# Kernel optimization log

Measured on AMD Instinct MI355X. Metric: run time of the kernel, lower is better.

The kernel has to match this reference:

```python
import jax, jax.numpy as jnp
import numpy as np

HIDDEN = 10

def setup_inputs() -> dict:
    key = jax.random.key(0)
    ks = jax.random.split(key, 12)
    B, T = 4096, 2048
    s_in = 1.0 / np.sqrt(HIDDEN)  # PyTorch RNN/Linear default init scale
    inp = {
        "x": jax.random.normal(ks[0], (B, T, 1), dtype=jnp.float32),
        "hidden_state": jax.random.normal(ks[1], (2, B, HIDDEN), dtype=jnp.float32),
        # layer 0 (input_size=1)
        "W_ih0": jax.random.uniform(ks[2], (HIDDEN, 1), jnp.float32, -s_in, s_in),
        "W_hh0": jax.random.uniform(ks[3], (HIDDEN, HIDDEN), jnp.float32, -s_in, s_in),
        "b_ih0": jax.random.uniform(ks[4], (HIDDEN,), jnp.float32, -s_in, s_in),
        "b_hh0": jax.random.uniform(ks[5], (HIDDEN,), jnp.float32, -s_in, s_in),
        # layer 1 (input_size=HIDDEN)
        "W_ih1": jax.random.uniform(ks[6], (HIDDEN, HIDDEN), jnp.float32, -s_in, s_in),
        "W_hh1": jax.random.uniform(ks[7], (HIDDEN, HIDDEN), jnp.float32, -s_in, s_in),
        "b_ih1": jax.random.uniform(ks[8], (HIDDEN,), jnp.float32, -s_in, s_in),
        "b_hh1": jax.random.uniform(ks[9], (HIDDEN,), jnp.float32, -s_in, s_in),
        # output Linear(10, 1)
        "W_out": jax.random.uniform(ks[10], (1, HIDDEN), jnp.float32, -s_in, s_in),
        "b_out": jax.random.uniform(ks[11], (1,), jnp.float32, -s_in, s_in),
    }
    return inp


def reference(x, hidden_state, W_ih0, W_hh0, b_ih0, b_hh0,
              W_ih1, W_hh1, b_ih1, b_hh1, W_out, b_out):
    # x: [B, T, 1]; hidden_state: [2, B, H]
    h0_init, h1_init = hidden_state[0], hidden_state[1]  # [B, H] each
    xs = jnp.swapaxes(x, 0, 1)  # [T, B, 1] for scan over time

    def step(carry, xt):
        h0, h1 = carry
        h0n = jnp.tanh(xt @ W_ih0.T + b_ih0 + h0 @ W_hh0.T + b_hh0)
        h1n = jnp.tanh(h0n @ W_ih1.T + b_ih1 + h1 @ W_hh1.T + b_hh1)
        return (h0n, h1n), h1n

    (h0_f, h1_f), ys = jax.lax.scan(step, (h0_init, h1_init), xs)  # ys: [T, B, H]
    rnn_output = jnp.swapaxes(ys, 0, 1)  # [B, T, H]
    outs = rnn_output @ W_out.T + b_out  # [B, T, 1] (fused per-timestep Linear)
    hidden_out = jnp.stack([h0_f, h1_f], axis=0)  # [2, B, H]
    return outs, hidden_out
```

## Files before the change

kernel.cpp:

```cpp
#include <hip/hip_runtime.h>

#define HID 10
#define TT  2048
#define BB  4096

typedef float f2 __attribute__((ext_vector_type(2)));

static __device__ __forceinline__ f2 pkmul(f2 a, f2 b) {
    f2 d; asm("v_pk_mul_f32 %0, %1, %2" : "=v"(d) : "v"(a), "v"(b)); return d;
}
static __device__ __forceinline__ f2 pkfma(f2 a, f2 b, f2 c) {
    f2 d; asm("v_pk_fma_f32 %0, %1, %2, %3" : "=v"(d) : "v"(a), "v"(b), "v"(c)); return d;
}

__device__ __forceinline__ float fast_tanh(float x) {
    float e = exp2f(x * 2.885390081777926814f);
    float r = __builtin_amdgcn_rcpf(e + 1.0f);
    return fmaf(-2.0f, r, 1.0f);
}

__global__ void __launch_bounds__(192) rnn_kernel(
    const float* __restrict__ x,    const float* __restrict__ hs,
    const float* __restrict__ Wih0, const float* __restrict__ Whh0,
    const float* __restrict__ bih0, const float* __restrict__ bhh0,
    const float* __restrict__ Wih1, const float* __restrict__ Whh1,
    const float* __restrict__ bih1, const float* __restrict__ bhh1,
    const float* __restrict__ Wout, const float* __restrict__ boutp,
    float* __restrict__ out)
{
    const int tid   = threadIdx.x;
    const int role  = tid >> 6;
    const int lane  = tid & 15;
    const int grp   = (tid >> 4) & 3;
    const int row   = blockIdx.x * 4 + grp;
    const bool act  = (lane < HID);
    const bool olane = (lane == HID);

    __shared__ float lds[4 * 272];
    float* h0r = &lds[grp * 272];
    float* ur  = h0r + 128;
    float* h1b = h0r + 256;

    const float* xrow = x   + (size_t)row * TT;
    float*       orow = out + (size_t)row * TT;

    f2 w0p[5]; float wih0i = 0.f, b0c = 0.f; f2 H0[5];
    float4 xq = make_float4(0,0,0,0);
    f2 w1p[5]; float ub = 0.f;
    f2 w2p[5]; f2 H1[5]; float bo = 0.f;
    float P1 = 0.f, P2 = 0.f, P3 = 0.f;
    float h0own = 0.f, h1own = 0.f;

    if (role == 0) {
        #pragma unroll
        for (int j = 0; j < 5; ++j)
            w0p[j] = act ? f2{Whh0[lane*HID + 2*j], Whh0[lane*HID + 2*j+1]}
                         : f2{0.f, 0.f};
        wih0i = act ? Wih0[lane] : 0.f;
        b0c   = act ? (bih0[lane] + bhh0[lane]) : 0.f;
        #pragma unroll
        for (int j = 0; j < 5; ++j)
            H0[j] = f2{hs[row*HID + 2*j], hs[row*HID + 2*j+1]};
        xq = *(const float4*)(xrow);
    } else if (role == 1) {
        #pragma unroll
        for (int j = 0; j < 5; ++j)
            w1p[j] = act ? f2{Wih1[lane*HID + 2*j], Wih1[lane*HID + 2*j+1]}
                         : f2{0.f, 0.f};
        ub = act ? (bih1[lane] + bhh1[lane]) : (olane ? boutp[0] : 0.f);
    } else {
        #pragma unroll
        for (int j = 0; j < 5; ++j)
            w2p[j] = act ? f2{Whh1[lane*HID + 2*j], Whh1[lane*HID + 2*j+1]}
                   : (olane ? f2{Wout[2*j], Wout[2*j+1]} : f2{0.f, 0.f});
        #pragma unroll
        for (int j = 0; j < 5; ++j)
            H1[j] = f2{hs[BB*HID + row*HID + 2*j], hs[BB*HID + row*HID + 2*j+1]};
        bo = boutp[0];
    }

    const int M = TT / 4;
    for (int m = 0; m <= M + 1; ++m) {
        if (role == 0) {
            if (m < M) {
                const int mn = (m + 1 < M) ? m + 1 : M - 1;
                const float4 xn = *(const float4*)(xrow + 4 * mn);
                const float xs[4] = {xq.x, xq.y, xq.z, xq.w};
                #pragma unroll
                for (int k = 0; k < 4; ++k) {
                    const int slot = ((4 * m + k) & 7) * 16;
                    f2 acc = pkmul(w0p[0], H0[0]);
                    acc = pkfma(w0p[1], H0[1], acc);
                    acc = pkfma(w0p[2], H0[2], acc);
                    acc = pkfma(w0p[3], H0[3], acc);
                    acc = pkfma(w0p[4], H0[4], acc);
                    const float a0 = fmaf(xs[k], wih0i, b0c);
                    h0own = fast_tanh((a0 + acc.x) + acc.y);
                    h0r[slot + lane] = h0own;
                    __builtin_amdgcn_wave_barrier();
                    const float* rb = h0r + slot;
                    const float4 r0 = *(const float4*)(rb);
                    const float4 r1 = *(const float4*)(rb + 4);
                    const f2     r2 = *(const f2*)(rb + 8);
                    H0[0] = f2{r0.x, r0.y}; H0[1] = f2{r0.z, r0.w};
                    H0[2] = f2{r1.x, r1.y}; H0[3] = f2{r1.z, r1.w};
                    H0[4] = r2;
                }
                xq = xn;
            }
        } else if (role == 1) {
            if (m >= 1 && m <= M) {
                const int tb = 4 * (m - 1);
                float4 a[4], b[4]; f2 c[4];
                #pragma unroll
                for (int k = 0; k < 4; ++k) {
                    const float* rb = h0r + ((tb + k) & 7) * 16;
                    a[k] = *(const float4*)(rb);
                    b[k] = *(const float4*)(rb + 4);
                    c[k] = *(const f2*)(rb + 8);
                }
                #pragma unroll
                for (int k = 0; k < 4; ++k) {
                    f2 pc = pkmul(w1p[0], f2{a[k].x, a[k].y});
                    pc = pkfma(w1p[1], f2{a[k].z, a[k].w}, pc);
                    pc = pkfma(w1p[2], f2{b[k].x, b[k].y}, pc);
                    pc = pkfma(w1p[3], f2{b[k].z, b[k].w}, pc);
                    pc = pkfma(w1p[4], c[k], pc);
                    ur[((tb + k) & 7) * 16 + lane] = (ub + pc.x) + pc.y;
                }
            }
        } else {
            if (m >= 2 && m <= M + 1) {
                const int tb = 4 * (m - 2);
                float uo[4];
                #pragma unroll
                for (int k = 0; k < 4; ++k)
                    uo[k] = ur[((tb + k) & 7) * 16 + lane];
                float c0 = 0.f, c1 = 0.f, c2 = 0.f, c3 = 0.f;
                #pragma unroll
                for (int k = 0; k < 4; ++k) {
                    f2 qc = pkmul(w2p[0], H1[0]);
                    qc = pkfma(w2p[1], H1[1], qc);
                    qc = pkfma(w2p[2], H1[2], qc);
                    qc = pkfma(w2p[3], H1[3], qc);
                    qc = pkfma(w2p[4], H1[4], qc);
                    const float s1 = (uo[k] + qc.x) + qc.y;
                    if      (k == 0) c0 = s1;
                    else if (k == 1) c1 = s1;
                    else if (k == 2) c2 = s1;
                    else             c3 = s1;
                    h1own = fast_tanh(s1);
                    h1b[lane] = h1own;
                    __builtin_amdgcn_wave_barrier();
                    const float4 q0 = *(const float4*)(h1b);
                    const float4 q1 = *(const float4*)(h1b + 4);
                    const f2     q2 = *(const f2*)(h1b + 8);
                    H1[0] = f2{q0.x, q0.y}; H1[1] = f2{q0.z, q0.w};
                    H1[2] = f2{q1.x, q1.y}; H1[3] = f2{q1.z, q1.w};
                    H1[4] = q2;
                }
                if (olane && m >= 3)
                    *(float4*)(orow + tb - 4) = make_float4(P1, P2, P3, c0);
                P1 = c1; P2 = c2; P3 = c3;
            }
        }
        __syncthreads();
    }

    if (role == 2) {
        f2 e = pkmul(w2p[0], H1[0]);
        e = pkfma(w2p[1], H1[1], e);
        e = pkfma(w2p[2], H1[2], e);
        e = pkfma(w2p[3], H1[3], e);
        e = pkfma(w2p[4], H1[4], e);
        if (olane)
            *(float4*)(orow + TT - 4) = make_float4(P1, P2, P3, (bo + e.x) + e.y);
        if (act)
            out[(size_t)BB*TT + (size_t)BB*HID + (size_t)row*HID + lane] = h1own;
    }
    if (role == 0 && act)
        out[(size_t)BB*TT + (size_t)row*HID + lane] = h0own;
}

extern "C" void kernel_launch(void* const* d_in, const int* in_sizes, int n_in,
                              void* d_out, int out_size, void* d_ws, size_t ws_size,
                              hipStream_t stream) {
    const float* x    = (const float*)d_in[0];
    const float* hs   = (const float*)d_in[1];
    const float* Wih0 = (const float*)d_in[2];
    const float* Whh0 = (const float*)d_in[3];
    const float* bih0 = (const float*)d_in[4];
    const float* bhh0 = (const float*)d_in[5];
    const float* Wih1 = (const float*)d_in[6];
    const float* Whh1 = (const float*)d_in[7];
    const float* bih1 = (const float*)d_in[8];
    const float* bhh1 = (const float*)d_in[9];
    const float* Wout = (const float*)d_in[10];
    const float* bout = (const float*)d_in[11];
    float* out = (float*)d_out;

    dim3 grid(BB / 4), block(192);
    hipLaunchKernelGGL(rnn_kernel, grid, block, 0, stream,
        x, hs, Wih0, Whh0, bih0, bhh0, Wih1, Whh1, bih1, bhh1, Wout, bout, out);
}
```

Baseline: 294.0 us.

## Broadcast recurrent hidden state via ds_bpermute and double the pipeline chunk

The serial recurrences in roles 0 and 2 now exchange the hidden vector across lanes with ds_bpermute, replacing the LDS store, wave barrier and vector reloads, and compute the matvec with scalar FMAs split into two chains. Each pipeline stage now handles 8 timesteps instead of 4, with a 16-slot ring buffer, which halves the number of block-wide __syncthreads. The cost is ten bpermute ops per step instead of one store plus three loads, and the packed FMAs are replaced by twice as many scalar FMAs on the critical path.

```diff
diff --git a/kernel.cpp b/kernel.cpp
--- a/kernel.cpp
+++ b/kernel.cpp
@@ -17,6 +17,10 @@
     float e = exp2f(x * 2.885390081777926814f);
     float r = __builtin_amdgcn_rcpf(e + 1.0f);
     return fmaf(-2.0f, r, 1.0f);
+}
+
+__device__ __forceinline__ float bperm(int idx, float v) {
+    return __int_as_float(__builtin_amdgcn_ds_bpermute(idx, __float_as_int(v)));
 }
 
 __global__ void __launch_bounds__(192) rnn_kernel(
@@ -36,32 +40,33 @@
     const bool act  = (lane < HID);
     const bool olane = (lane == HID);
 
-    __shared__ float lds[4 * 272];
-    float* h0r = &lds[grp * 272];
-    float* ur  = h0r + 128;
-    float* h1b = h0r + 256;
+    __shared__ float lds[4 * 528];
+    float* h0r = &lds[grp * 528];
+    float* ur  = h0r + 256;
+
+    int bpidx[HID];
+    #pragma unroll
+    for (int j = 0; j < HID; ++j) bpidx[j] = ((tid & 48) + j) * 4;
 
     const float* xrow = x   + (size_t)row * TT;
     float*       orow = out + (size_t)row * TT;
 
-    f2 w0p[5]; float wih0i = 0.f, b0c = 0.f; f2 H0[5];
-    float4 xq = make_float4(0,0,0,0);
+    float w0[HID], wih0i = 0.f, b0c = 0.f;
     f2 w1p[5]; float ub = 0.f;
-    f2 w2p[5]; f2 H1[5]; float bo = 0.f;
+    float w2[HID];
+    float hown = 0.f;
+    float4 xa = make_float4(0,0,0,0), xb = make_float4(0,0,0,0);
     float P1 = 0.f, P2 = 0.f, P3 = 0.f;
-    float h0own = 0.f, h1own = 0.f;
+    float obias = 0.f;
 
     if (role == 0) {
         #pragma unroll
-        for (int j = 0; j < 5; ++j)
-            w0p[j] = act ? f2{Whh0[lane*HID + 2*j], Whh0[lane*HID + 2*j+1]}
-                         : f2{0.f, 0.f};
+        for (int j = 0; j < HID; ++j) w0[j] = act ? Whh0[lane*HID + j] : 0.f;
         wih0i = act ? Wih0[lane] : 0.f;
         b0c   = act ? (bih0[lane] + bhh0[lane]) : 0.f;
-        #pragma unroll
-        for (int j = 0; j < 5; ++j)
-            H0[j] = f2{hs[row*HID + 2*j], hs[row*HID + 2*j+1]};
-        xq = *(const float4*)(xrow);
+        hown  = act ? hs[row*HID + lane] : 0.f;
+        xa = *(const float4*)(xrow);
+        xb = *(const float4*)(xrow + 4);
     } else if (role == 1) {
         #pragma unroll
         for (int j = 0; j < 5; ++j)
@@ -70,116 +75,128 @@
         ub = act ? (bih1[lane] + bhh1[lane]) : (olane ? boutp[0] : 0.f);
     } else {
         #pragma unroll
-        for (int j = 0; j < 5; ++j)
-            w2p[j] = act ? f2{Whh1[lane*HID + 2*j], Whh1[lane*HID + 2*j+1]}
-                   : (olane ? f2{Wout[2*j], Wout[2*j+1]} : f2{0.f, 0.f});
-        #pragma unroll
-        for (int j = 0; j < 5; ++j)
-            H1[j] = f2{hs[BB*HID + row*HID + 2*j], hs[BB*HID + row*HID + 2*j+1]};
-        bo = boutp[0];
+        for (int j = 0; j < HID; ++j)
+            w2[j] = act ? Whh1[lane*HID + j] : (olane ? Wout[j] : 0.f);
+        hown  = act ? hs[BB*HID + row*HID + lane] : 0.f;
+        obias = olane ? boutp[0] : 0.f;
     }
 
-    const int M = TT / 4;
+    const int M = TT / 8;
     for (int m = 0; m <= M + 1; ++m) {
         if (role == 0) {
             if (m < M) {
                 const int mn = (m + 1 < M) ? m + 1 : M - 1;
-                const float4 xn = *(const float4*)(xrow + 4 * mn);
-                const float xs[4] = {xq.x, xq.y, xq.z, xq.w};
-                #pragma unroll
-                for (int k = 0; k < 4; ++k) {
-                    const int slot = ((4 * m + k) & 7) * 16;
-                    f2 acc = pkmul(w0p[0], H0[0]);
-                    acc = pkfma(w0p[1], H0[1], acc);
-                    acc = pkfma(w0p[2], H0[2], acc);
-                    acc = pkfma(w0p[3], H0[3], acc);
-                    acc = pkfma(w0p[4], H0[4], acc);
-                    const float a0 = fmaf(xs[k], wih0i, b0c);
-                    h0own = fast_tanh((a0 + acc.x) + acc.y);
-                    h0r[slot + lane] = h0own;
-                    __builtin_amdgcn_wave_barrier();
-                    const float* rb = h0r + slot;
-                    const float4 r0 = *(const float4*)(rb);
-                    const float4 r1 = *(const float4*)(rb + 4);
-                    const f2     r2 = *(const f2*)(rb + 8);
-                    H0[0] = f2{r0.x, r0.y}; H0[1] = f2{r0.z, r0.w};
-                    H0[2] = f2{r1.x, r1.y}; H0[3] = f2{r1.z, r1.w};
-                    H0[4] = r2;
-                }
-                xq = xn;
+                const float4 xn0 = *(const float4*)(xrow + 8 * mn);
+                const float4 xn1 = *(const float4*)(xrow + 8 * mn + 4);
+                const float xs[8] = {xa.x, xa.y, xa.z, xa.w,
+                                     xb.x, xb.y, xb.z, xb.w};
+                #pragma unroll
+                for (int k = 0; k < 8; ++k) {
+                    float r0 = bperm(bpidx[0], hown);
+                    float r1 = bperm(bpidx[1], hown);
+                    float r2 = bperm(bpidx[2], hown);
+                    float r3 = bperm(bpidx[3], hown);
+                    float r4 = bperm(bpidx[4], hown);
+                    float r5 = bperm(bpidx[5], hown);
+                    float r6 = bperm(bpidx[6], hown);
+                    float r7 = bperm(bpidx[7], hown);
+                    float r8 = bperm(bpidx[8], hown);
+                    float r9 = bperm(bpidx[9], hown);
+                    float a = fmaf(xs[k], wih0i, b0c), b = 0.f;
+                    a = fmaf(w0[0], r0, a); b = fmaf(w0[1], r1, b);
+                    a = fmaf(w0[2], r2, a); b = fmaf(w0[3], r3, b);
+                    a = fmaf(w0[4], r4, a); b = fmaf(w0[5], r5, b);
+                    a = fmaf(w0[6], r6, a); b = fmaf(w0[7], r7, b);
+                    a = fmaf(w0[8], r8, a); b = fmaf(w0[9], r9, b);
+                    hown = fast_tanh(a + b);
+                    h0r[((8*m + k) & 15) * 16 + lane] = hown;
+                }
+                xa = xn0; xb = xn1;
             }
         } else if (role == 1) {
             if (m >= 1 && m <= M) {
-                const int tb = 4 * (m - 1);
-                float4 a[4], b[4]; f2 c[4];
-                #pragma unroll
-                for (int k = 0; k < 4; ++k) {
-                    const float* rb = h0r + ((tb + k) & 7) * 16;
-                    a[k] = *(const float4*)(rb);
-                    b[k] = *(const float4*)(rb + 4);
-                    c[k] = *(const f2*)(rb + 8);
-                }
-                #pragma unroll
-                for (int k = 0; k < 4; ++k) {
-                    f2 pc = pkmul(w1p[0], f2{a[k].x, a[k].y});
-                    pc = pkfma(w1p[1], f2{a[k].z, a[k].w}, pc);
-                    pc = pkfma(w1p[2], f2{b[k].x, b[k].y}, pc);
-                    pc = pkfma(w1p[3], f2{b[k].z, b[k].w}, pc);
-                    pc = pkfma(w1p[4], c[k], pc);
-                    ur[((tb + k) & 7) * 16 + lane] = (ub + pc.x) + pc.y;
+                const int tb = 8 * (m - 1);
+                #pragma unroll
+                for (int k = 0; k < 8; ++k) {
+                    const float* rb = h0r + ((tb + k) & 15) * 16;
+                    const f2 h0a = *(const f2*)(rb);
+                    const f2 h0b = *(const f2*)(rb + 2);
+                    const f2 h0c = *(const f2*)(rb + 4);
+                    const f2 h0d = *(const f2*)(rb + 6);
+                    const f2 h0e = *(const f2*)(rb + 8);
+                    f2 pc = pkmul(w1p[0], h0a);
+                    pc = pkfma(w1p[1], h0b, pc);
+                    pc = pkfma(w1p[2], h0c, pc);
+                    pc = pkfma(w1p[3], h0d, pc);
+                    pc = pkfma(w1p[4], h0e, pc);
+                    ur[((tb + k) & 15) * 16 + lane] = (ub + pc.x) + pc.y;
                 }
             }
         } else {
             if (m >= 2 && m <= M + 1) {
-                const int tb = 4 * (m - 2);
-                float uo[4];
-                #pragma unroll
-                for (int k = 0; k < 4; ++k)
-                    uo[k] = ur[((tb + k) & 7) * 16 + lane];
-                float c0 = 0.f, c1 = 0.f, c2 = 0.f, c3 = 0.f;
-                #pragma unroll
-                for (int k = 0; k < 4; ++k) {
-                    f2 qc = pkmul(w2p[0], H1[0]);
-                    qc = pkfma(w2p[1], H1[1], qc);
-                    qc = pkfma(w2p[2], H1[2], qc);
-                    qc = pkfma(w2p[3], H1[3], qc);
-                    qc = pkfma(w2p[4], H1[4], qc);
-                    const float s1 = (uo[k] + qc.x) + qc.y;
-                    if      (k == 0) c0 = s1;
-                    else if (k == 1) c1 = s1;
-                    else if (k == 2) c2 = s1;
-                    else             c3 = s1;
-                    h1own = fast_tanh(s1);
-                    h1b[lane] = h1own;
-                    __builtin_amdgcn_wave_barrier();
-                    const float4 q0 = *(const float4*)(h1b);
-                    const float4 q1 = *(const float4*)(h1b + 4);
-                    const f2     q2 = *(const f2*)(h1b + 8);
-                    H1[0] = f2{q0.x, q0.y}; H1[1] = f2{q0.z, q0.w};
-                    H1[2] = f2{q1.x, q1.y}; H1[3] = f2{q1.z, q1.w};
-                    H1[4] = q2;
-                }
-                if (olane && m >= 3)
-                    *(float4*)(orow + tb - 4) = make_float4(P1, P2, P3, c0);
-                P1 = c1; P2 = c2; P3 = c3;
+                const int tb = 8 * (m - 2);
+                float u[8];
+                #pragma unroll
+                for (int k = 0; k < 8; ++k)
+                    u[k] = ur[((tb + k) & 15) * 16 + lane];
+                float c[8];
+                #pragma unroll
+                for (int k = 0; k < 8; ++k) {
+                    float q0 = bperm(bpidx[0], hown);
+                    float q1 = bperm(bpidx[1], hown);
+                    float q2 = bperm(bpidx[2], hown);
+                    float q3 = bperm(bpidx[3], hown);
+                    float q4 = bperm(bpidx[4], hown);
+                    float q5 = bperm(bpidx[5], hown);
+                    float q6 = bperm(bpidx[6], hown);
+                    float q7 = bperm(bpidx[7], hown);
+                    float q8 = bperm(bpidx[8], hown);
+                    float q9 = bperm(bpidx[9], hown);
+                    float a = u[k], b = 0.f;
+                    a = fmaf(w2[0], q0, a); b = fmaf(w2[1], q1, b);
+                    a = fmaf(w2[2], q2, a); b = fmaf(w2[3], q3, b);
+                    a = fmaf(w2[4], q4, a); b = fmaf(w2[5], q5, b);
+                    a = fmaf(w2[6], q6, a); b = fmaf(w2[7], q7, b);
+                    a = fmaf(w2[8], q8, a); b = fmaf(w2[9], q9, b);
+                    const float s1 = a + b;
+                    c[k] = s1;
+                    hown = fast_tanh(s1);
+                }
+                if (olane) {
+                    if (m >= 3)
+                        *(float4*)(orow + tb - 4) = make_float4(P1, P2, P3, c[0]);
+                    *(float4*)(orow + tb) = make_float4(c[1], c[2], c[3], c[4]);
+                }
+                P1 = c[5]; P2 = c[6]; P3 = c[7];
             }
         }
         __syncthreads();
     }
 
     if (role == 2) {
-        f2 e = pkmul(w2p[0], H1[0]);
-        e = pkfma(w2p[1], H1[1], e);
-        e = pkfma(w2p[2], H1[2], e);
-        e = pkfma(w2p[3], H1[3], e);
-        e = pkfma(w2p[4], H1[4], e);
+        float q0 = bperm(bpidx[0], hown);
+        float q1 = bperm(bpidx[1], hown);
+        float q2 = bperm(bpidx[2], hown);
+        float q3 = bperm(bpidx[3], hown);
+        float q4 = bperm(bpidx[4], hown);
+        float q5 = bperm(bpidx[5], hown);
+        float q6 = bperm(bpidx[6], hown);
+        float q7 = bperm(bpidx[7], hown);
+        float q8 = bperm(bpidx[8], hown);
+        float q9 = bperm(bpidx[9], hown);
+        float a = obias, b = 0.f;
+        a = fmaf(w2[0], q0, a); b = fmaf(w2[1], q1, b);
+        a = fmaf(w2[2], q2, a); b = fmaf(w2[3], q3, b);
+        a = fmaf(w2[4], q4, a); b = fmaf(w2[5], q5, b);
+        a = fmaf(w2[6], q6, a); b = fmaf(w2[7], q7, b);
+        a = fmaf(w2[8], q8, a); b = fmaf(w2[9], q9, b);
         if (olane)
-            *(float4*)(orow + TT - 4) = make_float4(P1, P2, P3, (bo + e.x) + e.y);
+            *(float4*)(orow + TT - 4) = make_float4(P1, P2, P3, a + b);
         if (act)
-            out[(size_t)BB*TT + (size_t)BB*HID + (size_t)row*HID + lane] = h1own;
+            out[(size_t)BB*TT + (size_t)BB*HID + (size_t)row*HID + lane] = hown;
     }
     if (role == 0 && act)
-        out[(size_t)BB*TT + (size_t)row*HID + lane] = h0own;
+        out[(size_t)BB*TT + (size_t)row*HID + lane] = hown;
 }
 
 extern "C" void kernel_launch(void* const* d_in, const int* in_sizes, int n_in,
```

Measured after the change: 533.1 us. 81.3% more time.
